# Kernel tuning notes

Measured on AMD Instinct MI355X. Metric: run time of the kernel, lower is better.

The kernel has to match this reference:

```python
import jax, jax.numpy as jnp
import numpy as np

H = 1024  # hidden_size == input_size


def setup_inputs() -> dict:
    key = jax.random.key(0)
    ks = jax.random.split(key, 12)
    B, T, S, I = 64, 128, 256, 1024
    sc_in = 1.0 / np.sqrt(I)
    sc_h = 1.0 / np.sqrt(H)
    return {
        "trg_emb": jax.random.normal(ks[0], (B, T, I), jnp.float32),
        "h0": jax.random.normal(ks[1], (B, H), jnp.float32),
        "c0": jax.random.normal(ks[2], (B, H), jnp.float32),
        "ctx": jax.random.normal(ks[3], (B, S, H), jnp.float32),
        "src_len": jax.random.randint(ks[4], (B,), 1, S + 1, jnp.int32),
        # nn.LSTM params (gate order i, f, g, o)
        "W_ih": jax.random.uniform(ks[5], (4 * H, I), jnp.float32, -sc_h, sc_h),
        "W_hh": jax.random.uniform(ks[6], (4 * H, H), jnp.float32, -sc_h, sc_h),
        "b_ih": jax.random.uniform(ks[7], (4 * H,), jnp.float32, -sc_h, sc_h),
        "b_hh": jax.random.uniform(ks[8], (4 * H,), jnp.float32, -sc_h, sc_h),
        # GlobalAttention (Luong general): linear_in (H->H), linear_out (2H->H), no bias
        "W_in": jax.random.uniform(ks[9], (H, H), jnp.float32, -sc_h, sc_h),
        "W_out": jax.random.uniform(ks[10], (H, 2 * H), jnp.float32, -sc_h, sc_h),
    }


def _lstm_scan(trg_emb, h0, c0, W_ih, W_hh, b_ih, b_hh):
    # Precompute input contributions for all steps: [B,T,4H] -> scan over T
    x_gates = jnp.einsum('bti,gi->btg', trg_emb, W_ih) + b_ih + b_hh

    def step(carry, xg):
        h, c = carry
        gates = xg + h @ W_hh.T  # [B,4H]
        i, f, g, o = jnp.split(gates, 4, axis=-1)
        c = jax.nn.sigmoid(f) * c + jax.nn.sigmoid(i) * jnp.tanh(g)
        h = jax.nn.sigmoid(o) * jnp.tanh(c)
        return (h, c), h

    (hT, cT), hs = jax.lax.scan(step, (h0, c0), jnp.swapaxes(x_gates, 0, 1))
    return jnp.swapaxes(hs, 0, 1), hT, cT  # [B,T,H], [B,H], [B,H]


def reference(trg_emb, h0, c0, ctx, src_len, W_ih, W_hh, b_ih, b_hh, W_in, W_out):
    # input_feed=False: LSTM recurrence is independent of attention -> run once,
    # then batch the global attention over all T timesteps (same math as the loop).
    lstm_out, hT, cT = _lstm_scan(trg_emb, h0, c0, W_ih, W_hh, b_ih, b_hh)

    q = jnp.einsum('bth,gh->btg', lstm_out, W_in)          # linear_in
    scores = jnp.einsum('bth,bsh->bts', q, ctx)            # [B,T,S]
    mask = jnp.arange(ctx.shape[1])[None, None, :] < src_len[:, None, None]
    scores = jnp.where(mask, scores, -jnp.inf)
    attn = jax.nn.softmax(scores, axis=-1)                 # att_dropout=0
    context = jnp.einsum('bts,bsh->bth', attn, ctx)        # [B,T,H]
    h_tilde = jnp.tanh(
        jnp.einsum('btc,hc->bth', jnp.concatenate([context, lstm_out], axis=-1), W_out)
    )  # [B,T,H]
    return h_tilde, (hT[None], cT[None])
```

## Files before the change

kernel.cpp:

```cpp
#include <hip/hip_runtime.h>
#include <math.h>

#define BB 64
#define TT 128
#define SS 256
#define HHH 1024

typedef unsigned short u16;
typedef unsigned int u32;
typedef unsigned long long u64t;
typedef __bf16 bf16x8 __attribute__((ext_vector_type(8)));
typedef float f32x4 __attribute__((ext_vector_type(4)));
typedef u16 u16x8 __attribute__((ext_vector_type(8)));

__device__ __forceinline__ float sigmoidf_(float x) { return 1.0f / (1.0f + expf(-x)); }
__device__ __forceinline__ u16 f2bf(float f) {
    __bf16 h = (__bf16)f;
    return __builtin_bit_cast(u16, h);
}
__device__ __forceinline__ float b2f(u16 u) {
    return __builtin_bit_cast(float, (u32)u << 16);
}
template <typename OT>
__device__ __forceinline__ void stout(OT* p, float v) {
    if constexpr (sizeof(OT) == 2) *p = f2bf(v); else *p = v;
}
__device__ __forceinline__ void astore(u64t* p, u64t v) {
    __hip_atomic_store(p, v, __ATOMIC_RELAXED, __HIP_MEMORY_SCOPE_AGENT);
}
__device__ __forceinline__ int afetchadd(int* p) {
    return __hip_atomic_fetch_add(p, 1, __ATOMIC_RELAXED, __HIP_MEMORY_SCOPE_AGENT);
}
__device__ __forceinline__ int aload32(const int* p) {
    return __hip_atomic_load(p, __ATOMIC_RELAXED, __HIP_MEMORY_SCOPE_AGENT);
}
__device__ __forceinline__ void astore32(int* p, int v) {
    __hip_atomic_store(p, v, __ATOMIC_RELAXED, __HIP_MEMORY_SCOPE_AGENT);
}
#define GLOAD16(gsrc, ldst)                                                      \
    __builtin_amdgcn_global_load_lds(                                            \
        (const __attribute__((address_space(1))) unsigned int*)(const void*)(gsrc), \
        (__attribute__((address_space(3))) unsigned int*)(void*)(ldst), 16, 0, 0)

__global__ __launch_bounds__(256) void f32_to_bf16(const float* __restrict__ in,
                                                   u16* __restrict__ out, long n) {
    long i = ((long)blockIdx.x * 256 + threadIdx.x) * 8;
    float4 a = *(const float4*)(in + i);
    float4 b = *(const float4*)(in + i + 4);
    u16x8 o;
    o[0] = f2bf(a.x); o[1] = f2bf(a.y); o[2] = f2bf(a.z); o[3] = f2bf(a.w);
    o[4] = f2bf(b.x); o[5] = f2bf(b.y); o[6] = f2bf(b.z); o[7] = f2bf(b.w);
    *(u16x8*)(out + i) = o;
}

__global__ __launch_bounds__(128) void wfrag_build(const float* __restrict__ W,
                                                   u16* __restrict__ WF) {
    const int w = blockIdx.x, kq = blockIdx.y, bid = blockIdx.z;
    const int t = threadIdx.x;
    const int rh = t >> 6, lane = t & 63;
    const int rowp = bid * 32 + rh * 16 + (lane & 15);
    const int g = rowp & 3, jrow = rowp >> 2;
    const int k = kq * 256 + w * 32 + (lane >> 4) * 8;
    const float* src = W + ((size_t)(g * 1024 + jrow) << 10) + k;
    float4 v0 = *(const float4*)src;
    float4 v1 = *(const float4*)(src + 4);
    float vv[8] = {v0.x, v0.y, v0.z, v0.w, v1.x, v1.y, v1.z, v1.w};
    u16x8 hi, lo;
#pragma unroll
    for (int i = 0; i < 8; ++i) {
        u16 h = f2bf(vv[i]);
        hi[i] = h;
        lo[i] = f2bf(vv[i] - b2f(h));
    }
    size_t fr = ((((size_t)bid * 4 + kq) * 8 + w) * 2 + rh) * 2;
    *(u16x8*)(WF + fr * 512 + (size_t)lane * 8) = hi;
    *(u16x8*)(WF + (fr + 1) * 512 + (size_t)lane * 8) = lo;
}

__global__ __launch_bounds__(256) void h0frag(const float* __restrict__ h0,
                                              u16* __restrict__ slot) {
    int i = blockIdx.x * 256 + threadIdx.x;
    int b = i >> 7, jg = i & 127;
    int j = jg << 3;
    const float* src = h0 + ((size_t)b << 10) + j;
    float4 v0 = *(const float4*)src;
    float4 v1 = *(const float4*)(src + 4);
    float vv[8] = {v0.x, v0.y, v0.z, v0.w, v1.x, v1.y, v1.z, v1.w};
    u16x8 hi, lo;
#pragma unroll
    for (int e = 0; e < 8; ++e) {
        u16 h = f2bf(vv[e]);
        hi[e] = h;
        lo[e] = f2bf(vv[e] - b2f(h));
    }
    int g = b >> 4, bl = b & 15;
    int kq = j >> 8, w = (j >> 5) & 7, tr = (j >> 3) & 3;
    int lane = tr * 16 + bl;
    size_t base = (size_t)g * 32768 + (size_t)((kq * 8 + w) * 2) * 512 + (size_t)lane * 8;
    *(u16x8*)(slot + base) = hi;
    *(u16x8*)(slot + base + 512) = lo;
}

template <bool TANH, bool XGT, typename OT>
__global__ __launch_bounds__(256) void gemm_mfma_bt(
    const u16* __restrict__ A0, const u16* __restrict__ A1,
    const u16* __restrict__ B, OT* __restrict__ C,
    int M, int N, int K, int KA0,
    const float* __restrict__ bias0, const float* __restrict__ bias1)
{
    __shared__ uint4 As4[512];
    __shared__ uint4 Bs4[512];
    u16* As = (u16*)As4;
    u16* Bs = (u16*)Bs4;
    const int tid = threadIdx.x;
    const int l = tid & 63;
    const int w = tid >> 6;
    const int wm = w >> 1, wn = w & 1;
    const int tc = l & 15, tr8 = (l >> 4) << 3;
    const int m0 = blockIdx.y << 7, n0 = blockIdx.x << 7;
    f32x4 acc[4][4] = {};

    for (int k0 = 0; k0 < K; k0 += 32) {
        const u16* Ap = (k0 < KA0) ? A0 : A1;
        const int koff = (k0 < KA0) ? k0 : k0 - KA0;
#pragma unroll
        for (int r = 0; r < 2; ++r) {
            int u = tid + (r << 8);
            int row = u >> 2, q = u & 3;
            size_t arow;
            if (XGT) {
                int rr = m0 + row;
                arow = (size_t)((rr & 63) * 128 + (rr >> 6));
            } else {
                arow = (size_t)(m0 + row);
            }
            GLOAD16(Ap + arow * KA0 + koff + (q << 3), &As4[u]);
            GLOAD16(B + (size_t)(n0 + row) * K + k0 + (q << 3), &Bs4[u]);
        }
        __syncthreads();
        bf16x8 bfr[4];
#pragma unroll
        for (int j = 0; j < 4; ++j)
            bfr[j] = *(const bf16x8*)(Bs + ((wn << 6) + (j << 4) + tc) * 32 + tr8);
#pragma unroll
        for (int i = 0; i < 4; ++i) {
            bf16x8 af = *(const bf16x8*)(As + ((wm << 6) + (i << 4) + tc) * 32 + tr8);
#pragma unroll
            for (int j = 0; j < 4; ++j)
                acc[i][j] = __builtin_amdgcn_mfma_f32_16x16x32_bf16(af, bfr[j], acc[i][j], 0, 0, 0);
        }
        __syncthreads();
    }
#pragma unroll
    for (int j = 0; j < 4; ++j) {
        const int col = n0 + (wn << 6) + (j << 4) + tc;
        const float bias = XGT ? (bias0[col] + bias1[col]) : 0.0f;
#pragma unroll
        for (int i = 0; i < 4; ++i) {
#pragma unroll
            for (int v = 0; v < 4; ++v) {
                int r = m0 + (wm << 6) + (i << 4) + ((l >> 4) << 2) + v;
                float val = acc[i][j][v];
                if (XGT) {
                    int newr = ((col & 1023) << 2) | (col >> 10);
                    ((float*)C)[(size_t)(r >> 6) * 262144 + (size_t)newr * 64 + (r & 63)] = val + bias;
                } else {
                    if (TANH) val = tanhf(val);
                    stout(&C[(size_t)r * N + col], val);
                }
            }
        }
    }
}

__global__ __launch_bounds__(512) void lstm_scan8(
    const float* __restrict__ xgt, const u16* __restrict__ WF,
    const float* __restrict__ c0,
    const u16* __restrict__ h0s, u16* __restrict__ ring,
    float* __restrict__ hT, float* __restrict__ cT,
    u16* __restrict__ lstm16, int* __restrict__ bar)
{
    __shared__ float red[4][64][17];
    __shared__ __align__(8) u16 tileh[16][16];
    __shared__ __align__(8) u16 tilel[16][16];
    const int tid = threadIdx.x;
    const int bid = blockIdx.x;
    const int g = bid >> 6;
    const int ib = bid & 63;
    const int kg = tid >> 6, l = tid & 63;
    const int kq = kg & 3, rh = kg >> 2;
    const int j0 = ib << 4;
    const int ebl = tid & 15;
    const int ejl = tid >> 4;

    bf16x8 wfh[2][8], wfl[2][8];
#pragma unroll
    for (int rt = 0; rt < 2; ++rt) {
        const int R16 = ib * 4 + rh * 2 + rt;
        const int bw = R16 >> 1, rhw = R16 & 1;
#pragma unroll
        for (int w = 0; w < 8; ++w) {
            size_t fr = ((((size_t)bw * 4 + kq) * 8 + w) * 2 + rhw) * 2;
            wfh[rt][w] = *(const bf16x8*)(WF + fr * 512 + (size_t)l * 8);
            wfl[rt][w] = *(const bf16x8*)(WF + (fr + 1) * 512 + (size_t)l * 8);
        }
    }
    float cv = 0.0f;
    if (tid < 256) cv = c0[(size_t)(g * 16 + ebl) * 1024 + j0 + ejl];

    float xgv[4] = {};
    if (tid < 256) {
#pragma unroll
        for (int g2 = 0; g2 < 4; ++g2)
            xgv[g2] = xgt[(size_t)(((j0 + ejl) << 2) + g2) * 64 + g * 16 + ebl];
    }

    const int kqs = ib >> 4, ws = (ib >> 1) & 7;
    int* const gbar = bar + (g << 9);

    for (int t = 0; t < 128; ++t) {
        const u16* hin = ((t == 0) ? h0s : (ring + (size_t)(t - 1) * 131072)) + (size_t)g * 32768;
        u16* hout = ring + (size_t)t * 131072 + (size_t)g * 32768;

        f32x4 acc[2] = {};
        bf16x8 hbA[2], hbB[2];
#define LDW(HB, W)                                                                  \
        {                                                                           \
            size_t fb = (size_t)((kq * 8 + (W)) * 2) * 512 + (size_t)l * 8;         \
            HB[0] = *(const bf16x8*)(hin + fb);                                     \
            HB[1] = *(const bf16x8*)(hin + fb + 512);                               \
        }
        LDW(hbA, 0)
#pragma unroll
        for (int w = 0; w < 8; w += 2) {
            LDW(hbB, w + 1)
#pragma unroll
            for (int rt = 0; rt < 2; ++rt) {
                acc[rt] = __builtin_amdgcn_mfma_f32_16x16x32_bf16(wfh[rt][w], hbA[0], acc[rt], 0, 0, 0);
                acc[rt] = __builtin_amdgcn_mfma_f32_16x16x32_bf16(wfh[rt][w], hbA[1], acc[rt], 0, 0, 0);
                acc[rt] = __builtin_amdgcn_mfma_f32_16x16x32_bf16(wfl[rt][w], hbA[0], acc[rt], 0, 0, 0);
            }
            if (w + 2 < 8) LDW(hbA, w + 2)
#pragma unroll
            for (int rt = 0; rt < 2; ++rt) {
                acc[rt] = __builtin_amdgcn_mfma_f32_16x16x32_bf16(wfh[rt][w + 1], hbB[0], acc[rt], 0, 0, 0);
                acc[rt] = __builtin_amdgcn_mfma_f32_16x16x32_bf16(wfh[rt][w + 1], hbB[1], acc[rt], 0, 0, 0);
                acc[rt] = __builtin_amdgcn_mfma_f32_16x16x32_bf16(wfl[rt][w + 1], hbB[0], acc[rt], 0, 0, 0);
            }
        }
#undef LDW

#pragma unroll
        for (int rt = 0; rt < 2; ++rt)
#pragma unroll
            for (int v = 0; v < 4; ++v)
                red[kq][(rh << 5) + (rt << 4) + ((l >> 4) << 2) + v][l & 15] = acc[rt][v];
        __syncthreads();

        if (tid < 256) {
            float gate[4];
#pragma unroll
            for (int g2 = 0; g2 < 4; ++g2) {
                int rr = (ejl << 2) + g2;
                gate[g2] = red[0][rr][ebl] + red[1][rr][ebl] +
                           red[2][rr][ebl] + red[3][rr][ebl] + xgv[g2];
            }
            float ii = sigmoidf_(gate[0]);
            float ff = sigmoidf_(gate[1]);
            float gg = tanhf(gate[2]);
            float oo = sigmoidf_(gate[3]);
            float cn = ff * cv + ii * gg;
            float hn = oo * tanhf(cn);
            cv = cn;
            u16 hh = f2bf(hn);
            tileh[ebl][ejl] = hh;
            tilel[ebl][ejl] = f2bf(hn - b2f(hh));
            if (t == 127) {
                hT[(size_t)(g * 16 + ebl) * 1024 + j0 + ejl] = hn;
                cT[(size_t)(g * 16 + ebl) * 1024 + j0 + ejl] = cn;
            }
        }
        __syncthreads();

        if (tid < 128) {
            const int plane = tid >> 6, rem = tid & 63;
            const int b2 = rem >> 2, half = (rem >> 1) & 1, qq = rem & 1;
            const int lane = ((ib & 1) * 2 + half) * 16 + b2;
            const u16* tp = plane ? &tilel[b2][half * 8 + qq * 4] : &tileh[b2][half * 8 + qq * 4];
            size_t a16 = (size_t)(((kqs * 8 + ws) * 2 + plane)) * 512 + (size_t)lane * 8 + qq * 4;
            astore((u64t*)(hout + a16), *(const u64t*)tp);
            if (plane == 0) {
                int qj = rem & 3;
                *(u64t*)(lstm16 + ((size_t)(g * 16 + b2) * 128 + t) * 1024 + j0 + qj * 4) =
                    *(const u64t*)&tileh[b2][qj * 4];
            }
        }

        if (t < 127) {
            if (tid < 256) {
#pragma unroll
                for (int g2 = 0; g2 < 4; ++g2)
                    xgv[g2] = xgt[(size_t)(t + 1) * 262144 +
                                  (size_t)(((j0 + ejl) << 2) + g2) * 64 + g * 16 + ebl];
            }
            __syncthreads();
            if (tid == 0) {
                const int leaf = ib & 7;
                int a = afetchadd(&gbar[leaf * 16]);
                if ((a & 7) == 7) {
                    int r = afetchadd(&gbar[128]);
                    if ((r & 7) == 7) astore32(&gbar[136], t + 1);
                    while (aload32(&gbar[136]) < t + 1) __builtin_amdgcn_s_sleep(2);
                    astore32(&gbar[144 + leaf * 16], t + 1);
                } else {
                    while (aload32(&gbar[144 + leaf * 16]) < t + 1)
                        __builtin_amdgcn_s_sleep(2);
                }
            }
            __syncthreads();
        }
    }
}

__global__ __launch_bounds__(256) void scores_mfma(
    const float* __restrict__ q, const float* __restrict__ ctx,
    float* __restrict__ C)
{
    __shared__ u16 Ahi[4096], Alo[4096], Bhi[4096], Blo[4096];
    const int tid = threadIdx.x;
    const int l = tid & 63, w = tid >> 6;
    const int wm = w >> 1, wn = w & 1;
    const int tc = l & 15, tr8 = (l >> 4) << 3;
    const int b = blockIdx.z, n0 = blockIdx.x << 7;
    const float* A = q + (size_t)b * 131072;
    const float* B = ctx + (size_t)b * 262144;
    f32x4 acc[4][4] = {};

    for (int k0 = 0; k0 < 1024; k0 += 32) {
#pragma unroll
        for (int r = 0; r < 4; ++r) {
            int flat = r * 256 + tid;
            int row = flat >> 3, kq = (flat & 7) << 2;
            int o = row * 32 + kq;
            float4 va = *(const float4*)(A + (size_t)row * 1024 + k0 + kq);
            u16 a0 = f2bf(va.x), a1 = f2bf(va.y), a2 = f2bf(va.z), a3 = f2bf(va.w);
            *(ushort4*)&Ahi[o] = (ushort4){a0, a1, a2, a3};
            *(ushort4*)&Alo[o] = (ushort4){f2bf(va.x - b2f(a0)), f2bf(va.y - b2f(a1)),
                                           f2bf(va.z - b2f(a2)), f2bf(va.w - b2f(a3))};
            float4 vb = *(const float4*)(B + (size_t)(n0 + row) * 1024 + k0 + kq);
            u16 g0 = f2bf(vb.x), g1 = f2bf(vb.y), g2 = f2bf(vb.z), g3 = f2bf(vb.w);
            *(ushort4*)&Bhi[o] = (ushort4){g0, g1, g2, g3};
            *(ushort4*)&Blo[o] = (ushort4){f2bf(vb.x - b2f(g0)), f2bf(vb.y - b2f(g1)),
                                           f2bf(vb.z - b2f(g2)), f2bf(vb.w - b2f(g3))};
        }
        __syncthreads();
        bf16x8 bh[4], bl[4];
#pragma unroll
        for (int j = 0; j < 4; ++j) {
            int o = ((wn << 6) + (j << 4) + tc) * 32 + tr8;
            bh[j] = *(const bf16x8*)(Bhi + o);
            bl[j] = *(const bf16x8*)(Blo + o);
        }
#pragma unroll
        for (int i = 0; i < 4; ++i) {
            int o = ((wm << 6) + (i << 4) + tc) * 32 + tr8;
            bf16x8 ah = *(const bf16x8*)(Ahi + o);
            bf16x8 al = *(const bf16x8*)(Alo + o);
#pragma unroll
            for (int j = 0; j < 4; ++j) {
                acc[i][j] = __builtin_amdgcn_mfma_f32_16x16x32_bf16(ah, bh[j], acc[i][j], 0, 0, 0);
                acc[i][j] = __builtin_amdgcn_mfma_f32_16x16x32_bf16(ah, bl[j], acc[i][j], 0, 0, 0);
                acc[i][j] = __builtin_amdgcn_mfma_f32_16x16x32_bf16(al, bh[j], acc[i][j], 0, 0, 0);
            }
        }
        __syncthreads();
    }
#pragma unroll
    for (int j = 0; j < 4; ++j) {
        int col = n0 + (wn << 6) + (j << 4) + tc;
#pragma unroll
        for (int i = 0; i < 4; ++i)
#pragma unroll
            for (int v = 0; v < 4; ++v) {
                int r = (wm << 6) + (i << 4) + ((l >> 4) << 2) + v;
                C[(size_t)b * 32768 + (size_t)r * 256 + col] = acc[i][j][v];
            }
    }
}

__global__ __launch_bounds__(256) void softmax_mask16(
    const float* __restrict__ scores, const int* __restrict__ src_len,
    u16* __restrict__ attn16)
{
    __shared__ float red[4];
    const int b = blockIdx.y, t = blockIdx.x, s = threadIdx.x;
    const float* row = scores + ((long)b * TT + t) * SS;
    const int L = src_len[b];
    float v = (s < L) ? row[s] : -INFINITY;
    float m = v;
#pragma unroll
    for (int o = 32; o >= 1; o >>= 1) m = fmaxf(m, __shfl_xor(m, o));
    if ((s & 63) == 0) red[s >> 6] = m;
    __syncthreads();
    m = fmaxf(fmaxf(red[0], red[1]), fmaxf(red[2], red[3]));
    __syncthreads();
    float e = (s < L) ? expf(v - m) : 0.0f;
    float sum = e;
#pragma unroll
    for (int o = 32; o >= 1; o >>= 1) sum += __shfl_xor(sum, o);
    if ((s & 63) == 0) red[s >> 6] = sum;
    __syncthreads();
    sum = red[0] + red[1] + red[2] + red[3];
    attn16[((long)b * TT + t) * SS + s] = f2bf(e / sum);
}

__global__ __launch_bounds__(256) void ctxattn_mfma(
    const u16* __restrict__ attn16, const float* __restrict__ ctx,
    u16* __restrict__ ctxout16)
{
    __shared__ u16 As[4096];
    __shared__ u16 Bs[128][40];
    const int tid = threadIdx.x;
    const int l = tid & 63, w = tid >> 6;
    const int wm = w >> 1, wn = w & 1;
    const int tc = l & 15, tr8 = (l >> 4) << 3;
    const int b = blockIdx.z, n0 = blockIdx.x << 7;
    f32x4 acc[4][4] = {};

    for (int k0 = 0; k0 < 256; k0 += 32) {
        {
            int row = tid >> 1, off = (tid & 1) << 4;
            const u16* src = attn16 + (size_t)b * 32768 + (size_t)row * 256 + k0 + off;
            *(uint4*)&As[row * 32 + off] = *(const uint4*)src;
            *(uint4*)&As[row * 32 + off + 8] = *(const uint4*)(src + 8);
        }
#pragma unroll
        for (int p = 0; p < 4; ++p) {
            int flat = p * 256 + tid;
            int s = flat >> 5, hc = flat & 31;
            float4 v = *(const float4*)(ctx + (size_t)b * 262144 +
                                        (size_t)(k0 + s) * 1024 + n0 + (hc << 2));
            Bs[(hc << 2) + 0][s] = f2bf(v.x);
            Bs[(hc << 2) + 1][s] = f2bf(v.y);
            Bs[(hc << 2) + 2][s] = f2bf(v.z);
            Bs[(hc << 2) + 3][s] = f2bf(v.w);
        }
        __syncthreads();
        bf16x8 bfr[4];
#pragma unroll
        for (int j = 0; j < 4; ++j)
            bfr[j] = *(const bf16x8*)&Bs[(wn << 6) + (j << 4) + tc][tr8];
#pragma unroll
        for (int i = 0; i < 4; ++i) {
            bf16x8 af = *(const bf16x8*)(As + ((wm << 6) + (i << 4) + tc) * 32 + tr8);
#pragma unroll
            for (int j = 0; j < 4; ++j)
                acc[i][j] = __builtin_amdgcn_mfma_f32_16x16x32_bf16(af, bfr[j], acc[i][j], 0, 0, 0);
        }
        __syncthreads();
    }
#pragma unroll
    for (int j = 0; j < 4; ++j) {
        int col = n0 + (wn << 6) + (j << 4) + tc;
#pragma unroll
        for (int i = 0; i < 4; ++i)
#pragma unroll
            for (int v = 0; v < 4; ++v) {
                int r = (wm << 6) + (i << 4) + ((l >> 4) << 2) + v;
                ctxout16[((size_t)b * 128 + r) * 1024 + col] = f2bf(acc[i][j][v]);
            }
    }
}

extern "C" void kernel_launch(void* const* d_in, const int* in_sizes, int n_in,
                              void* d_out, int out_size, void* d_ws, size_t ws_size,
                              hipStream_t stream)
{
    const float* trg_emb = (const float*)d_in[0];
    const float* h0      = (const float*)d_in[1];
    const float* c0      = (const float*)d_in[2];
    const float* ctx     = (const float*)d_in[3];
    const int*   src_len = (const int*)d_in[4];
    const float* W_ih    = (const float*)d_in[5];
    const float* W_hh    = (const float*)d_in[6];
    const float* b_ih    = (const float*)d_in[7];
    const float* b_hh    = (const float*)d_in[8];
    const float* W_in    = (const float*)d_in[9];
    const float* W_out   = (const float*)d_in[10];

    float* out = (float*)d_out;
    float* h_tilde = out;
    float* hT = out + (size_t)BB * TT * HHH;
    float* cT = hT + (size_t)BB * HHH;

    char* w = (char*)d_ws;
    auto take = [&](size_t bytes) { void* p = w; w += (bytes + 255) & ~(size_t)255; return p; };
    char* base0 = w;
    u16* trg16  = (u16*)take(8388608ull * 2);
    u16* Wih16  = (u16*)take(4194304ull * 2);
    take(8388608ull);
    u16* ring   = (u16*)base0;
    u16* h0s    = (u16*)take(262144ull);
    u16* Win16  = (u16*)take(1048576ull * 2);
    u16* Wout16 = (u16*)take(2097152ull * 2);
    u16* lstm16 = (u16*)take(8388608ull * 2);
    u16* WF     = (u16*)take(16777216ull);
    int* bar    = (int*)take(8192);
    char* regionB = w;
    float* xgt = (float*)take(33554432ull * 4);
    float* q        = (float*)regionB;
    float* scores   = (float*)(regionB + 33554432ull);
    u16*   attn16   = (u16*)(regionB + 41943040ull);
    u16*   ctxout16 = (u16*)(regionB + 46137344ull);

    hipMemsetAsync(bar, 0, 8192, stream);

    f32_to_bf16<<<4096, 256, 0, stream>>>(trg_emb, trg16, 8388608);
    f32_to_bf16<<<2048, 256, 0, stream>>>(W_ih, Wih16, 4194304);
    f32_to_bf16<<<512, 256, 0, stream>>>(W_in, Win16, 1048576);
    f32_to_bf16<<<1024, 256, 0, stream>>>(W_out, Wout16, 2097152);
    wfrag_build<<<dim3(8, 4, 128), 128, 0, stream>>>(W_hh, WF);
    h0frag<<<32, 256, 0, stream>>>(h0, h0s);

    gemm_mfma_bt<false, true, float><<<dim3(32, 64), 256, 0, stream>>>(
        trg16, trg16, Wih16, xgt, 8192, 4096, 1024, 1024, b_ih, b_hh);

    lstm_scan8<<<256, 512, 0, stream>>>(xgt, WF, c0, h0s, ring,
                                        hT, cT, lstm16, bar);

    gemm_mfma_bt<false, false, float><<<dim3(8, 64), 256, 0, stream>>>(
        lstm16, lstm16, Win16, q, 8192, 1024, 1024, 1024, nullptr, nullptr);

    scores_mfma<<<dim3(2, 1, 64), 256, 0, stream>>>(q, ctx, scores);

    softmax_mask16<<<dim3(TT, BB, 1), 256, 0, stream>>>(scores, src_len, attn16);

    ctxattn_mfma<<<dim3(8, 1, 64), 256, 0, stream>>>(attn16, ctx, ctxout16);

    gemm_mfma_bt<true, false, float><<<dim3(8, 64), 256, 0, stream>>>(
        ctxout16, lstm16, Wout16, h_tilde, 8192, 1024, 2048, 1024, nullptr, nullptr);
}
```

Measured before the change: 1.004 ms.

## Store LSTM input gates row-major and merge fp32-to-bf16 conversions into one launch

The input-projection GEMM now writes gates in plain [t*64+b][4H] row-major order with the bias folded in, replacing the scattered transposed xgt store whose writes were poorly coalesced. The scan kernel's per-step prefetch indexing and thread mapping are changed to read the new layout, with the gate index on contiguous threads. The four separate conversion launches become a single kernel, and the grid-barrier spin sleep is shortened. The scan's per-step loads become strided across batch rows instead of fully contiguous, which may cost some read efficiency on the latency-critical path.

```diff
diff --git a/kernel.cpp b/kernel.cpp
--- a/kernel.cpp
+++ b/kernel.cpp
@@ -42,14 +42,26 @@
         (const __attribute__((address_space(1))) unsigned int*)(const void*)(gsrc), \
         (__attribute__((address_space(3))) unsigned int*)(void*)(ldst), 16, 0, 0)
 
-__global__ __launch_bounds__(256) void f32_to_bf16(const float* __restrict__ in,
-                                                   u16* __restrict__ out, long n) {
-    long i = ((long)blockIdx.x * 256 + threadIdx.x) * 8;
+__global__ __launch_bounds__(256) void convert_all(
+    const float* __restrict__ trg, const float* __restrict__ wih,
+    const float* __restrict__ win, const float* __restrict__ wout,
+    u16* __restrict__ trg16, u16* __restrict__ wih16,
+    u16* __restrict__ win16, u16* __restrict__ wout16)
+{
+    int b = blockIdx.x;
+    const float* in;
+    u16* out;
+    long base;
+    if (b < 4096)      { in = trg;  out = trg16;  base = (long)b * 2048; }
+    else if (b < 6144) { in = wih;  out = wih16;  base = (long)(b - 4096) * 2048; }
+    else if (b < 6656) { in = win;  out = win16;  base = (long)(b - 6144) * 2048; }
+    else               { in = wout; out = wout16; base = (long)(b - 6656) * 2048; }
+    long i = base + (long)threadIdx.x * 8;
     float4 a = *(const float4*)(in + i);
-    float4 b = *(const float4*)(in + i + 4);
+    float4 c = *(const float4*)(in + i + 4);
     u16x8 o;
     o[0] = f2bf(a.x); o[1] = f2bf(a.y); o[2] = f2bf(a.z); o[3] = f2bf(a.w);
-    o[4] = f2bf(b.x); o[5] = f2bf(b.y); o[6] = f2bf(b.z); o[7] = f2bf(b.w);
+    o[4] = f2bf(c.x); o[5] = f2bf(c.y); o[6] = f2bf(c.z); o[7] = f2bf(c.w);
     *(u16x8*)(out + i) = o;
 }
 
@@ -101,7 +113,7 @@
     *(u16x8*)(slot + base + 512) = lo;
 }
 
-template <bool TANH, bool XGT, typename OT>
+template <bool TANH, bool AREMAP, bool BIAS, typename OT>
 __global__ __launch_bounds__(256) void gemm_mfma_bt(
     const u16* __restrict__ A0, const u16* __restrict__ A1,
     const u16* __restrict__ B, OT* __restrict__ C,
@@ -128,7 +140,7 @@
             int u = tid + (r << 8);
             int row = u >> 2, q = u & 3;
             size_t arow;
-            if (XGT) {
+            if (AREMAP) {
                 int rr = m0 + row;
                 arow = (size_t)((rr & 63) * 128 + (rr >> 6));
             } else {
@@ -154,27 +166,22 @@
 #pragma unroll
     for (int j = 0; j < 4; ++j) {
         const int col = n0 + (wn << 6) + (j << 4) + tc;
-        const float bias = XGT ? (bias0[col] + bias1[col]) : 0.0f;
+        const float bias = BIAS ? (bias0[col] + bias1[col]) : 0.0f;
 #pragma unroll
         for (int i = 0; i < 4; ++i) {
 #pragma unroll
             for (int v = 0; v < 4; ++v) {
                 int r = m0 + (wm << 6) + (i << 4) + ((l >> 4) << 2) + v;
-                float val = acc[i][j][v];
-                if (XGT) {
-                    int newr = ((col & 1023) << 2) | (col >> 10);
-                    ((float*)C)[(size_t)(r >> 6) * 262144 + (size_t)newr * 64 + (r & 63)] = val + bias;
-                } else {
-                    if (TANH) val = tanhf(val);
-                    stout(&C[(size_t)r * N + col], val);
-                }
-            }
-        }
-    }
-}
-
-__global__ __launch_bounds__(512) void lstm_scan8(
-    const float* __restrict__ xgt, const u16* __restrict__ WF,
+                float val = acc[i][j][v] + bias;
+                if (TANH) val = tanhf(val);
+                stout(&C[(size_t)r * N + col], val);
+            }
+        }
+    }
+}
+
+__global__ __launch_bounds__(512) void lstm_scan9(
+    const float* __restrict__ xg, const u16* __restrict__ WF,
     const float* __restrict__ c0,
     const u16* __restrict__ h0s, u16* __restrict__ ring,
     float* __restrict__ hT, float* __restrict__ cT,
@@ -190,8 +197,8 @@
     const int kg = tid >> 6, l = tid & 63;
     const int kq = kg & 3, rh = kg >> 2;
     const int j0 = ib << 4;
-    const int ebl = tid & 15;
-    const int ejl = tid >> 4;
+    const int ejl = tid & 15;
+    const int ebl = (tid >> 4) & 15;
 
     bf16x8 wfh[2][8], wfl[2][8];
 #pragma unroll
@@ -212,7 +219,7 @@
     if (tid < 256) {
 #pragma unroll
         for (int g2 = 0; g2 < 4; ++g2)
-            xgv[g2] = xgt[(size_t)(((j0 + ejl) << 2) + g2) * 64 + g * 16 + ebl];
+            xgv[g2] = xg[(size_t)(g * 16 + ebl) * 4096 + (size_t)(g2 << 10) + j0 + ejl];
     }
 
     const int kqs = ib >> 4, ws = (ib >> 1) & 7;
@@ -300,8 +307,8 @@
             if (tid < 256) {
 #pragma unroll
                 for (int g2 = 0; g2 < 4; ++g2)
-                    xgv[g2] = xgt[(size_t)(t + 1) * 262144 +
-                                  (size_t)(((j0 + ejl) << 2) + g2) * 64 + g * 16 + ebl];
+                    xgv[g2] = xg[(size_t)((t + 1) * 64 + g * 16 + ebl) * 4096 +
+                                 (size_t)(g2 << 10) + j0 + ejl];
             }
             __syncthreads();
             if (tid == 0) {
@@ -310,11 +317,11 @@
                 if ((a & 7) == 7) {
                     int r = afetchadd(&gbar[128]);
                     if ((r & 7) == 7) astore32(&gbar[136], t + 1);
-                    while (aload32(&gbar[136]) < t + 1) __builtin_amdgcn_s_sleep(2);
+                    while (aload32(&gbar[136]) < t + 1) __builtin_amdgcn_s_sleep(1);
                     astore32(&gbar[144 + leaf * 16], t + 1);
                 } else {
                     while (aload32(&gbar[144 + leaf * 16]) < t + 1)
-                        __builtin_amdgcn_s_sleep(2);
+                        __builtin_amdgcn_s_sleep(1);
                 }
             }
             __syncthreads();
@@ -507,7 +514,7 @@
     u16* WF     = (u16*)take(16777216ull);
     int* bar    = (int*)take(8192);
     char* regionB = w;
-    float* xgt = (float*)take(33554432ull * 4);
+    float* xg = (float*)take(33554432ull * 4);
     float* q        = (float*)regionB;
     float* scores   = (float*)(regionB + 33554432ull);
     u16*   attn16   = (u16*)(regionB + 41943040ull);
@@ -515,20 +522,18 @@
 
     hipMemsetAsync(bar, 0, 8192, stream);
 
-    f32_to_bf16<<<4096, 256, 0, stream>>>(trg_emb, trg16, 8388608);
-    f32_to_bf16<<<2048, 256, 0, stream>>>(W_ih, Wih16, 4194304);
-    f32_to_bf16<<<512, 256, 0, stream>>>(W_in, Win16, 1048576);
-    f32_to_bf16<<<1024, 256, 0, stream>>>(W_out, Wout16, 2097152);
+    convert_all<<<7680, 256, 0, stream>>>(trg_emb, W_ih, W_in, W_out,
+                                          trg16, Wih16, Win16, Wout16);
     wfrag_build<<<dim3(8, 4, 128), 128, 0, stream>>>(W_hh, WF);
     h0frag<<<32, 256, 0, stream>>>(h0, h0s);
 
-    gemm_mfma_bt<false, true, float><<<dim3(32, 64), 256, 0, stream>>>(
-        trg16, trg16, Wih16, xgt, 8192, 4096, 1024, 1024, b_ih, b_hh);
-
-    lstm_scan8<<<256, 512, 0, stream>>>(xgt, WF, c0, h0s, ring,
+    gemm_mfma_bt<false, true, true, float><<<dim3(32, 64), 256, 0, stream>>>(
+        trg16, trg16, Wih16, xg, 8192, 4096, 1024, 1024, b_ih, b_hh);
+
+    lstm_scan9<<<256, 512, 0, stream>>>(xg, WF, c0, h0s, ring,
                                         hT, cT, lstm16, bar);
 
-    gemm_mfma_bt<false, false, float><<<dim3(8, 64), 256, 0, stream>>>(
+    gemm_mfma_bt<false, false, false, float><<<dim3(8, 64), 256, 0, stream>>>(
         lstm16, lstm16, Win16, q, 8192, 1024, 1024, 1024, nullptr, nullptr);
 
     scores_mfma<<<dim3(2, 1, 64), 256, 0, stream>>>(q, ctx, scores);
@@ -537,6 +542,6 @@
 
     ctxattn_mfma<<<dim3(8, 1, 64), 256, 0, stream>>>(attn16, ctx, ctxout16);
 
-    gemm_mfma_bt<true, false, float><<<dim3(8, 64), 256, 0, stream>>>(
+    gemm_mfma_bt<true, false, false, float><<<dim3(8, 64), 256, 0, stream>>>(
         ctxout16, lstm16, Wout16, h_tilde, 8192, 1024, 2048, 1024, nullptr, nullptr);
 }
```

After: 1.026 ms. 1.02x slower.
